# Performance work log

Measured on AMD Instinct MI355X. Metric: run time of the kernel, lower is better.

## Reference

```python
import jax, jax.numpy as jnp
import numpy as np
import math

H = 32          # num heads
D_NOPE = 128
D_ROPE = 64
D_QK = D_NOPE + D_ROPE   # 192
D_V = 128
KV_LORA = 512
EPS = 1e-6
ROPE_THETA = 10000.0
FACTOR = 40.0
BETA_FAST, BETA_SLOW = 32.0, 1.0
ORIG_MAX_POS = 4096
MSCALE_ALL_DIM = 1.0


def _yarn_inv_freq():
    dim = D_ROPE
    pos_freqs = ROPE_THETA ** (np.arange(0, dim, 2, dtype=np.float64) / dim)
    inv_extra = 1.0 / pos_freqs
    inv_inter = 1.0 / (FACTOR * pos_freqs)

    def corr_dim(n_rot):
        return dim * math.log(ORIG_MAX_POS / (n_rot * 2 * math.pi)) / (2 * math.log(ROPE_THETA))
    low = max(math.floor(corr_dim(BETA_FAST)), 0)
    high = min(math.ceil(corr_dim(BETA_SLOW)), dim - 1)
    ramp = np.clip((np.arange(dim // 2, dtype=np.float64) - low) / max(high - low, 1e-3), 0, 1)
    inv_freq_mask = 1.0 - ramp  # extrapolation_factor = 1
    inv_freq = inv_inter * (1 - inv_freq_mask) + inv_extra * inv_freq_mask
    return jnp.asarray(inv_freq, dtype=jnp.float32)  # [D_ROPE//2]


def _apply_rope_gptj(x, cos, sin):
    # x: [T, n, D_ROPE]; cos/sin: [T, D_ROPE//2]; interleaved (is_neox_style=False)
    x2 = x.reshape(*x.shape[:-1], D_ROPE // 2, 2)
    x1, xo = x2[..., 0], x2[..., 1]
    c = cos[:, None, :]
    s = sin[:, None, :]
    r1 = x1 * c - xo * s
    r2 = xo * c + x1 * s
    return jnp.stack([r1, r2], axis=-1).reshape(x.shape)


def _rmsnorm(x, w):
    var = jnp.mean(x.astype(jnp.float32) ** 2, axis=-1, keepdims=True)
    return (x * jax.lax.rsqrt(var + EPS)) * w


def setup_inputs() -> dict:
    key = jax.random.key(0)
    ks = jax.random.split(key, 8)
    T, HID = 2048, 4096
    def w(k, shape, fan_in):
        return jax.random.normal(k, shape, dtype=jnp.float32) * (1.0 / math.sqrt(fan_in))
    return {
        "positions": jnp.arange(T, dtype=jnp.int32),
        "hidden_states": jax.random.normal(ks[0], (T, HID), dtype=jnp.float32),
        "Wqa": w(ks[1], (HID, 1536), HID),
        "q_a_ln": jnp.ones((1536,), dtype=jnp.float32),
        "Wqb": w(ks[2], (1536, H * D_QK), 1536),
        "Wkva": w(ks[3], (HID, KV_LORA + D_ROPE), HID),
        "kv_a_ln": jnp.ones((KV_LORA,), dtype=jnp.float32),
        "Wkvb": w(ks[4], (KV_LORA, H * (D_NOPE + D_V)), KV_LORA),
        "Wo": w(ks[5], (H * D_V, HID), H * D_V),
    }


def reference(positions, hidden_states, Wqa, q_a_ln, Wqb, Wkva, kv_a_ln, Wkvb, Wo):
    T = hidden_states.shape[0]
    # softmax scaling with yarn mscale correction
    mscale = 0.1 * MSCALE_ALL_DIM * math.log(FACTOR) + 1.0
    scaling = (D_QK ** -0.5) * mscale * mscale

    # --- low-rank Q path ---
    q = hidden_states @ Wqa                       # [T, 1536]
    q = _rmsnorm(q, q_a_ln)
    q = (q @ Wqb).reshape(T, H, D_QK)             # [T, H, 192]
    q_nope, q_pe = q[..., :D_NOPE], q[..., D_NOPE:]

    # --- low-rank latent KV path ---
    latent = hidden_states @ Wkva                 # [T, 576]
    kv_a = _rmsnorm(latent[:, :KV_LORA], kv_a_ln) # [T, 512]
    k_pe = latent[:, None, KV_LORA:]              # [T, 1, 64]
    kv = (kv_a @ Wkvb).reshape(T, H, D_NOPE + D_V)
    k_nope = kv[..., :D_NOPE]                     # [T, H, 128]
    v = kv[..., D_NOPE:]                          # [T, H, 128]

    # --- decoupled RoPE on rope slice only ---
    inv_freq = _yarn_inv_freq()
    freqs = positions.astype(jnp.float32)[:, None] * inv_freq[None, :]  # [T, 32]
    cos, sin = jnp.cos(freqs), jnp.sin(freqs)
    q_pe = _apply_rope_gptj(q_pe, cos, sin)       # [T, H, 64]
    k_pe = _apply_rope_gptj(k_pe, cos, sin)       # [T, 1, 64]

    q = jnp.concatenate([q_nope, q_pe], axis=-1)                      # [T, H, 192]
    k = jnp.concatenate([k_nope, jnp.broadcast_to(k_pe, (T, H, D_ROPE))], axis=-1)

    # --- causal MHA over assembled K/V ---
    scores = jnp.einsum('thd,shd->hts', q, k) * scaling               # [H, T, T]
    causal = positions[None, :, None] >= positions[None, None, :]
    scores = jnp.where(causal, scores, jnp.finfo(scores.dtype).min)
    probs = jax.nn.softmax(scores, axis=-1)
    attn = jnp.einsum('hts,shd->thd', probs, v).reshape(T, H * D_V)
    return attn @ Wo                                                   # [T, 4096]
```

## Files before the change

### kernel.cpp

```cpp
#include <hip/hip_runtime.h>
#include <math.h>

typedef __bf16 bf16x8 __attribute__((ext_vector_type(8)));
typedef float f32x4 __attribute__((ext_vector_type(4)));
typedef unsigned short u16;
typedef unsigned int u32;

#define T_SEQ 2048
#define NHEAD 32

__device__ __forceinline__ u16 f2bu(float f){
  u32 u = __float_as_uint(f);
  u32 r = (u + 0x7fffu + ((u >> 16) & 1u)) >> 16;
  return (u16)r;
}

__device__ __forceinline__ void gload_lds16(const void* g, void* l){
  __builtin_amdgcn_global_load_lds((const __attribute__((address_space(1))) u32*)g,
                                   (__attribute__((address_space(3))) u32*)l, 16, 0, 0);
}

__global__ void cast_f32_bf16(const float* __restrict__ in, u16* __restrict__ out, int n4){
  int i = blockIdx.x * blockDim.x + threadIdx.x;
  int stride = gridDim.x * blockDim.x;
// ... 20 lines not shown
  __syncthreads();
  #pragma unroll
  for (int i = 0; i < 16; i++){
    int nr = lr * 16 + i;
    dst[(size_t)(n0 + nr) * K + k0 + lc] = f2bu(tile[lc][nr]);
  }
}

__global__ void rope_table(const int* __restrict__ positions, float* __restrict__ cosT,
                           float* __restrict__ sinT, float lo, float denom){
  int idx = blockIdx.x * blockDim.x + threadIdx.x;
  if (idx >= T_SEQ * 32) return;
  int t = idx >> 5, i = idx & 31;
  float pf = powf(10000.f, (float)i / 32.f);
  float inv_extra = 1.f / pf;
  float inv_inter = 1.f / (40.f * pf);
  float ramp = fminf(fmaxf(((float)i - lo) / denom, 0.f), 1.f);
  float invf = inv_inter * ramp + inv_extra * (1.f - ramp);
  float fr = (float)positions[t] * invf;
  cosT[idx] = cosf(fr);
  sinT[idx] = sinf(fr);
}

__global__ void rmsnorm_cast(const float* __restrict__ in, int istride, int n,
                             const float* __restrict__ w, u16* __restrict__ out, int ostride){
  int row = blockIdx.x;
  const float* x = in + (size_t)row * istride;
  float ss = 0.f;
  for (int c = threadIdx.x; c < n; c += blockDim.x){ float v = x[c]; ss += v * v; }
  #pragma unroll
  for (int off = 1; off < 64; off <<= 1) ss += __shfl_xor(ss, off);
  __shared__ float wsum[4];
  if ((threadIdx.x & 63) == 0) wsum[threadIdx.x >> 6] = ss;
  __syncthreads();
  float tot = wsum[0] + wsum[1] + wsum[2] + wsum[3];
  float scale = rsqrtf(tot / (float)n + 1e-6f);
  for (int c = threadIdx.x; c < n; c += blockDim.x)
    out[(size_t)row * ostride + c] = f2bu(x[c] * scale * w[c]);
}

__global__ void rope_kpe(const float* __restrict__ lat, int lstride, int loff,
                         const float* __restrict__ cosT,
                         const float* __restrict__ sinT, u16* __restrict__ kpe){
  int idx = blockIdx.x * blockDim.x + threadIdx.x;
  if (idx >= T_SEQ * 32) return;
  int t = idx >> 5, i = idx & 31;
  float x1 = lat[(size_t)t * lstride + loff + 2 * i];
  float x2 = lat[(size_t)t * lstride + loff + 2 * i + 1];
  float c = cosT[idx], s = sinT[idx];
  kpe[t * 64 + 2 * i]     = f2bu(x1 * c - x2 * s);
  kpe[t * 64 + 2 * i + 1] = f2bu(x2 * c + x1 * s);
}

__global__ void kpe_bcast(const u16* __restrict__ kpe, u16* __restrict__ Kp){
  int idx = blockIdx.x * blockDim.x + threadIdx.x;
  if (idx >= NHEAD * T_SEQ * 16) return;
  int h = idx >> 15;
  int rem = idx & 32767;
  int t = rem >> 4, j = rem & 15;
  ushort4 v = ((const ushort4*)(kpe + t * 64))[j];
  ((ushort4*)(Kp + (size_t)h * T_SEQ * 192 + (size_t)t * 192 + 128))[j] = v;
}

__global__ void build_vt(const u16* __restrict__ Vtmp, u16* __restrict__ Vt){
  __shared__ u16 tile[128][72];
  int t0 = blockIdx.x * 64;
  int h = blockIdx.y;
  #pragma unroll
  for (int i = 0; i < 32; i++){
    int lin = threadIdx.x + i * 256;
    int tt = lin >> 7, dd = lin & 127;
    tile[dd][tt] = Vtmp[(size_t)(t0 + tt) * 4096 + h * 128 + dd];
  }
  __syncthreads();
  #pragma unroll
  for (int i = 0; i < 32; i++){
    int lin = threadIdx.x + i * 256;
    int dd = lin >> 6, tt = lin & 63;
    Vt[(size_t)(h * 128 + dd) * T_SEQ + t0 + tt] = tile[dd][tt];
  }
}

template<int EPI>
__global__ __launch_bounds__(256) void gemm_bt(const u16* __restrict__ A, const u16* __restrict__ BT,
                                               float* __restrict__ C, u16* __restrict__ O1,
                                               u16* __restrict__ O2,
                                               const float* __restrict__ cosT,
                                               const float* __restrict__ sinT,
                                               float scaling, int M, int N, int K){
  __shared__ __align__(1024) char lds[32768];
  const int tid = threadIdx.x;
  const int wave = tid >> 6, lane = tid & 63;
  const int lg = lane >> 4, lm = lane & 15;

  int gx = gridDim.x;
  int nwg = gx * gridDim.y;
  int orig = blockIdx.y * gx + blockIdx.x;
  int qq = nwg >> 3, rr = nwg & 7, xc = orig & 7, rest = orig >> 3;
  int wg = (xc < rr ? xc * (qq + 1) : rr * (qq + 1) + (xc - rr) * qq) + rest;
  const int bn = (wg % gx) * 128, bm = (wg / gx) * 128;

  const int wr = (wave >> 1) * 64, wc = (wave & 1) * 64;
  f32x4 acc[4][4] = {};
  int srow[2], scol[2], soff[2];
  #pragma unroll
  for (int j = 0; j < 2; j++){
    int o = (wave * 2 + j) * 1024 + lane * 16;
    int row = o >> 6;
    int cg = ((o >> 4) & 3) ^ ((row >> 1) & 3);
    srow[j] = row; scol[j] = cg * 8; soff[j] = (wave * 2 + j) * 1024;
  }

  #pragma unroll
  for (int j = 0; j < 2; j++){
    gload_lds16(A  + (size_t)(bm + srow[j]) * K + scol[j], lds + soff[j]);
    gload_lds16(BT + (size_t)(bn + srow[j]) * K + scol[j], lds + 16384 + soff[j]);
  }

  int cur = 0;
  for (int k0 = 0; k0 < K; k0 += 32){
    if (k0 + 32 < K){
      char* dA = lds + (cur ^ 1) * 8192;
      char* dB = lds + 16384 + (cur ^ 1) * 8192;
      #pragma unroll
      for (int j = 0; j < 2; j++){
        gload_lds16(A  + (size_t)(bm + srow[j]) * K + k0 + 32 + scol[j], dA + soff[j]);
        gload_lds16(BT + (size_t)(bn + srow[j]) * K + k0 + 32 + scol[j], dB + soff[j]);
      }
      asm volatile("s_waitcnt vmcnt(4)" ::: "memory");
    } else {
      asm volatile("s_waitcnt vmcnt(0)" ::: "memory");
    }
    __builtin_amdgcn_sched_barrier(0);
    __builtin_amdgcn_s_barrier();

    const char* ldsA = lds + cur * 8192;
    const char* ldsB = lds + 16384 + cur * 8192;
    bf16x8 af[4], bfr[4];
    #pragma unroll
    for (int m = 0; m < 4; m++){
      int r = wr + m * 16 + lm;
      af[m] = *(const bf16x8*)(ldsA + r * 64 + ((lg ^ ((r >> 1) & 3)) << 4));
    }
    #pragma unroll
    for (int n = 0; n < 4; n++){
      int r = wc + n * 16 + lm;
      bfr[n] = *(const bf16x8*)(ldsB + r * 64 + ((lg ^ ((r >> 1) & 3)) << 4));
    }
    __builtin_amdgcn_s_setprio(1);
    #pragma unroll
    for (int m = 0; m < 4; m++)
      #pragma unroll
      for (int n = 0; n < 4; n++)
        acc[m][n] = __builtin_amdgcn_mfma_f32_16x16x32_bf16(af[m], bfr[n], acc[m][n], 0, 0, 0);
    __builtin_amdgcn_s_setprio(0);
    __builtin_amdgcn_s_barrier();
    cur ^= 1;
  }

  #pragma unroll
  for (int m = 0; m < 4; m++)
    #pragma unroll
    for (int n = 0; n < 4; n++)
      #pragma unroll
      for (int q = 0; q < 4; q++){
        int r = bm + wr + m * 16 + lg * 4 + q;
        int c = bn + wc + n * 16 + lm;
        float v = acc[m][n][q];
        if (EPI == 0){
          C[(size_t)r * N + c] = v;
        } else if (EPI == 1){
          float vp = __shfl_xor(v, 1);
          int h = c / 192, d = c - h * 192;
          float outv;
          if (d < 128) outv = v;
          else {
            int i = (d - 128) >> 1;
            float co = cosT[r * 32 + i], si = sinT[r * 32 + i];
            outv = (d & 1) ? (v * co + vp * si) : (v * co - vp * si);
          }
          O1[(size_t)h * T_SEQ * 192 + (size_t)r * 192 + d] = f2bu(outv * scaling);
        } else {
          int h = c >> 8, d = c & 255;
          if (d < 128) O1[(size_t)h * T_SEQ * 192 + (size_t)r * 192 + d] = f2bu(v);
          else         O2[(size_t)r * 4096 + h * 128 + (d - 128)] = f2bu(v);
        }
      }
}

__global__ __launch_bounds__(512, 1) void flash_attn(const u16* __restrict__ Qp, const u16* __restrict__ Kp,
                                                     const u16* __restrict__ Vt, u16* __restrict__ attnb){
  const int b = blockIdx.x;
  const int h = (b & 7) + 8 * ((b >> 3) & 3);
  const int s = b >> 5;
  const int tid = threadIdx.x;
  const int wave = tid >> 6, lane = tid & 63;
  const int lg = lane >> 4, lm = lane & 15;

  __shared__ __align__(1024) char lds[100352];
  char* ldsK = lds;
  char* ldsV = lds + 49152;
  u16*  Pw   = (u16*)(lds + 81920 + wave * 2304);

  const u16* KpH = Kp + (size_t)h * T_SEQ * 192;
  const u16* VtH = Vt + (size_t)h * 128 * T_SEQ;

  int kO[3], kSrc[3];
  #pragma unroll
  for (int j = 0; j < 3; j++){
    int o = (tid + 512 * j) * 16;
    int r = o / 384, c = (o % 384) >> 4;
    kO[j] = o; kSrc[j] = r * 192 + ((c ^ (r & 7)) << 3);
  }
  int vO[2], vSrc[2];
  #pragma unroll
  for (int j = 0; j < 2; j++){
    int o = (tid + 512 * j) * 16;
    int d = o >> 7, c = (o & 127) >> 4;
    vO[j] = o; vSrc[j] = d * T_SEQ + ((c ^ (d & 7)) << 3);
  }

  #pragma unroll 1
  for (int rep = 0; rep < 2; rep++){
    const int qt = rep ? s : (15 - s);
    const int qbase = qt * 128 + wave * 16;
    const int nt = 2 * qt + 2;

    __syncthreads();

    bf16x8 qf[6];
    const u16* Qbase = Qp + (size_t)(h * T_SEQ + qbase + lm) * 192 + lg * 8;
    #pragma unroll
    for (int dk = 0; dk < 6; dk++) qf[dk] = *(const bf16x8*)(Qbase + dk * 32);

    f32x4 o_[8] = {};
    float m_[4], l_[4];
    #pragma unroll
    for (int q = 0; q < 4; q++){ m_[q] = -3.0e38f; l_[q] = 0.f; }

    #pragma unroll
    for (int j = 0; j < 3; j++) gload_lds16(KpH + kSrc[j], ldsK + kO[j]);
    #pragma unroll
    for (int j = 0; j < 2; j++) gload_lds16(VtH + vSrc[j], ldsV + vO[j]);

    for (int kt = 0; kt < nt; kt++){
      const int t0 = kt * 64;
      const int bsel = kt & 1;
      asm volatile("s_waitcnt vmcnt(0)" ::: "memory");
      __builtin_amdgcn_sched_barrier(0);
      __builtin_amdgcn_s_barrier();
      if (kt + 1 < nt){
        const int t1 = t0 + 64;
        char* Kd = ldsK + (bsel ^ 1) * 24576;
        char* Vd = ldsV + (bsel ^ 1) * 16384;
        #pragma unroll
        for (int j = 0; j < 3; j++) gload_lds16(KpH + (size_t)t1 * 192 + kSrc[j], Kd + kO[j]);
        #pragma unroll
        for (int j = 0; j < 2; j++) gload_lds16(VtH + vSrc[j] + t1, Vd + vO[j]);
      }
      const char* Kb = ldsK + bsel * 24576;
      const char* Vb = ldsV + bsel * 16384;

      f32x4 s_[4] = {};
      __builtin_amdgcn_s_setprio(1);
      #pragma unroll
      for (int hh = 0; hh < 4; hh++){
        const int r = hh * 16 + lm;
        const int rb = r * 384, rx = r & 7;
        #pragma unroll
        for (int dk = 0; dk < 6; dk++){
          bf16x8 kf = *(const bf16x8*)(Kb + rb + (((dk * 4 + lg) ^ rx) << 4));
          s_[hh] = __builtin_amdgcn_mfma_f32_16x16x32_bf16(qf[dk], kf, s_[hh], 0, 0, 0);
        }
      }
      __builtin_amdgcn_s_setprio(0);
      #pragma unroll
      for (int hh = 0; hh < 4; hh++)
        #pragma unroll
        for (int q = 0; q < 4; q++){
          int col = t0 + hh * 16 + lm;
          int qrow = qbase + lg * 4 + q;
          if (col > qrow) s_[hh][q] = -3.0e38f;
        }
      float pm[4];
      #pragma unroll
      for (int q = 0; q < 4; q++)
        pm[q] = fmaxf(fmaxf(s_[0][q], s_[1][q]), fmaxf(s_[2][q], s_[3][q]));
      int ok = (pm[0] <= m_[0] + 8.f) & (pm[1] <= m_[1] + 8.f) &
               (pm[2] <= m_[2] + 8.f) & (pm[3] <= m_[3] + 8.f);
      if (!__all(ok)){
        #pragma unroll
        for (int q = 0; q < 4; q++){
          float v = pm[q];
          #pragma unroll
          for (int off = 8; off; off >>= 1) v = fmaxf(v, __shfl_xor(v, off));
          float mn = fmaxf(m_[q], v);
          float alpha = (m_[q] <= -1.0e37f) ? 0.f : __expf(m_[q] - mn);
          l_[q] *= alpha;
          #pragma unroll
          for (int n = 0; n < 8; n++) o_[n][q] *= alpha;
          m_[q] = mn;
        }
      }
      #pragma unroll
      for (int q = 0; q < 4; q++){
        #pragma unroll
        for (int hh = 0; hh < 4; hh++){
          float p = __expf(s_[hh][q] - m_[q]);
          l_[q] += p;
          Pw[(lg * 4 + q) * 72 + hh * 16 + lm] = f2bu(p);
        }
      }
      asm volatile("s_waitcnt lgkmcnt(0)" ::: "memory");
      __builtin_amdgcn_sched_barrier(0);
      __builtin_amdgcn_s_setprio(1);
      #pragma unroll
      for (int ks = 0; ks < 2; ks++){
        bf16x8 pf = *(const bf16x8*)((const char*)Pw + lm * 144 + ks * 64 + lg * 16);
        #pragma unroll
        for (int n = 0; n < 8; n++){
          const int d = n * 16 + lm;
          bf16x8 vf = *(const bf16x8*)(Vb + d * 128 + (((ks * 4 + lg) ^ (d & 7)) << 4));
          o_[n] = __builtin_amdgcn_mfma_f32_16x16x32_bf16(pf, vf, o_[n], 0, 0, 0);
        }
      }
      __builtin_amdgcn_s_setprio(0);
    }

    #pragma unroll
    for (int q = 0; q < 4; q++){
      #pragma unroll
      for (int off = 8; off; off >>= 1) l_[q] += __shfl_xor(l_[q], off);
    }
    float inv[4];
    #pragma unroll
    for (int q = 0; q < 4; q++) inv[q] = 1.f / l_[q];
    #pragma unroll
    for (int n = 0; n < 8; n++)
      #pragma unroll
      for (int q = 0; q < 4; q++){
        int r = qbase + lg * 4 + q;
        attnb[(size_t)r * 4096 + h * 128 + n * 16 + lm] = f2bu(o_[n][q] * inv[q]);
      }
  }
}

extern "C" void kernel_launch(void* const* d_in, const int* in_sizes, int n_in,
                              void* d_out, int out_size, void* d_ws, size_t ws_size,
                              hipStream_t stream){
  const int*   positions = (const int*)d_in[0];
  const float* hidden    = (const float*)d_in[1];
  const float* Wqa       = (const float*)d_in[2];
  const float* q_a_ln    = (const float*)d_in[3];
  const float* Wqb       = (const float*)d_in[4];
  const float* Wkva      = (const float*)d_in[5];
  const float* kv_a_ln   = (const float*)d_in[6];
  const float* Wkvb      = (const float*)d_in[7];
  const float* Wo        = (const float*)d_in[8];
  float* out = (float*)d_out;
  char* ws = (char*)d_ws;

  const size_t o_hid  = 0;
  const size_t o_cos  = 16777216;
  const size_t o_sin  = 17039360;
  const size_t o_comb = 17301504;
  const size_t o_qln  = 35127296;
  const size_t o_kva  = 41418752;
  const size_t o_kpe  = 43515904;
  const size_t o_W    = 43778048;
  const size_t o_Qp   = 77332480;
  const size_t o_Kp   = 102498304;
  const size_t o_Vtmp = 127664128;
  const size_t o_Vt   = 144441344;
  const size_t o_att  = 161218560;

  u16*   hidB = (u16*)(ws + o_hid);
  float* cosT = (float*)(ws + o_cos);
  float* sinT = (float*)(ws + o_sin);
  float* comb = (float*)(ws + o_comb);
  u16*   qln  = (u16*)(ws + o_qln);
  u16*   kva  = (u16*)(ws + o_kva);
  u16*   kpe  = (u16*)(ws + o_kpe);
  u16*   Wt   = (u16*)(ws + o_W);
  u16*   Qp   = (u16*)(ws + o_Qp);
  u16*   Kp   = (u16*)(ws + o_Kp);
  u16*   Vtmp = (u16*)(ws + o_Vtmp);
  u16*   Vt   = (u16*)(ws + o_Vt);
  u16*   attnb= (u16*)(ws + o_att);

  double mscale = 0.1 * log(40.0) + 1.0;
  float scaling = (float)(pow(192.0, -0.5) * mscale * mscale);
  const double PI = 3.14159265358979323846;
  double cd_fast = 64.0 * log(4096.0 / (32.0 * 2.0 * PI)) / (2.0 * log(10000.0));
  double cd_slow = 64.0 * log(4096.0 / ( 1.0 * 2.0 * PI)) / (2.0 * log(10000.0));
  double lo_d = fmax(floor(cd_fast), 0.0);
  double hi_d = fmin(ceil(cd_slow), 63.0);
  float lo = (float)lo_d;
  float denom = (float)fmax(hi_d - lo_d, 0.001);

  cast_f32_bf16<<<2048, 256, 0, stream>>>(hidden, hidB, T_SEQ * 4096 / 4);
  rope_table<<<256, 256, 0, stream>>>(positions, cosT, sinT, lo, denom);
  transpose_cast<<<dim3(4096 / 64, 1536 / 64), 256, 0, stream>>>(Wqa, Wt, 4096, 1536);
  transpose_cast<<<dim3(4096 / 64, 640 / 64), 256, 0, stream>>>(Wkva, Wt + (size_t)1536 * 4096, 4096, 576);
  gemm_bt<0><<<dim3(2176 / 128, 2048 / 128), 256, 0, stream>>>(hidB, Wt, comb, nullptr, nullptr,
                                                               nullptr, nullptr, 0.f, 2048, 2176, 4096);
  rmsnorm_cast<<<2048, 256, 0, stream>>>(comb, 2176, 1536, q_a_ln, qln, 1536);
  rmsnorm_cast<<<2048, 256, 0, stream>>>(comb + 1536, 2176, 512, kv_a_ln, kva, 512);
  rope_kpe<<<256, 256, 0, stream>>>(comb, 2176, 2048, cosT, sinT, kpe);
  transpose_cast<<<dim3(1536 / 64, 6144 / 64), 256, 0, stream>>>(Wqb, Wt, 1536, 6144);
  gemm_bt<1><<<dim3(6144 / 128, 2048 / 128), 256, 0, stream>>>(qln, Wt, nullptr, Qp, nullptr,
                                                               cosT, sinT, scaling, 2048, 6144, 1536);
  transpose_cast<<<dim3(512 / 64, 8192 / 64), 256, 0, stream>>>(Wkvb, Wt, 512, 8192);
  gemm_bt<2><<<dim3(8192 / 128, 2048 / 128), 256, 0, stream>>>(kva, Wt, nullptr, Kp, Vtmp,
                                                               nullptr, nullptr, 0.f, 2048, 8192, 512);
  kpe_bcast<<<NHEAD * T_SEQ * 16 / 256, 256, 0, stream>>>(kpe, Kp);
  build_vt<<<dim3(T_SEQ / 64, NHEAD), 256, 0, stream>>>(Vtmp, Vt);
  flash_attn<<<256, 512, 0, stream>>>(Qp, Kp, Vt, attnb);
  transpose_cast<<<dim3(4096 / 64, 4096 / 64), 256, 0, stream>>>(Wo, Wt, 4096, 4096);
  gemm_bt<0><<<dim3(4096 / 128, 2048 / 128), 256, 0, stream>>>(attnb, Wt, out, nullptr, nullptr,
                                                               nullptr, nullptr, 0.f, 2048, 4096, 4096);
}
```

Measured before the change: 441.8 us.

## Enlarge GEMM tiles to 256x256 with 8 waves and 64-deep K steps

Rewrites the shared GEMM kernel to use 256x256 output tiles with 512 threads (8 waves, each 128x64), K steps of 64, and a 128 KB double-buffered LDS with an XOR swizzle. Each K step is split into four phases that interleave the next tile's global-to-LDS loads with MFMA work. The goal is more data reuse per byte loaded and fewer loop iterations and barriers. The trade-offs are fewer workgroups (e.g. 64–128 tiles for the smaller GEMMs on a 256-CU part), much higher LDS and register use, and a padded kv_a projection width (2176 to 2304), which shifts the workspace offsets.

```diff
diff --git a/kernel.cpp b/kernel.cpp
--- a/kernel.cpp
+++ b/kernel.cpp
@@ -126,91 +126,117 @@
 }
 
 template<int EPI>
-__global__ __launch_bounds__(256) void gemm_bt(const u16* __restrict__ A, const u16* __restrict__ BT,
-                                               float* __restrict__ C, u16* __restrict__ O1,
-                                               u16* __restrict__ O2,
-                                               const float* __restrict__ cosT,
-                                               const float* __restrict__ sinT,
-                                               float scaling, int M, int N, int K){
-  __shared__ __align__(1024) char lds[32768];
+__global__ __launch_bounds__(512, 2) void gemm_bt(const u16* __restrict__ A, const u16* __restrict__ BT,
+                                                  float* __restrict__ C, u16* __restrict__ O1,
+                                                  u16* __restrict__ O2,
+                                                  const float* __restrict__ cosT,
+                                                  const float* __restrict__ sinT,
+                                                  float scaling, int M, int N, int K){
+  __shared__ __align__(1024) char lds[131072];
   const int tid = threadIdx.x;
   const int wave = tid >> 6, lane = tid & 63;
   const int lg = lane >> 4, lm = lane & 15;
+  const int wm = wave >> 2, wn = wave & 3;
 
   int gx = gridDim.x;
   int nwg = gx * gridDim.y;
   int orig = blockIdx.y * gx + blockIdx.x;
-  int qq = nwg >> 3, rr = nwg & 7, xc = orig & 7, rest = orig >> 3;
-  int wg = (xc < rr ? xc * (qq + 1) : rr * (qq + 1) + (xc - rr) * qq) + rest;
-  const int bn = (wg % gx) * 128, bm = (wg / gx) * 128;
-
-  const int wr = (wave >> 1) * 64, wc = (wave & 1) * 64;
-  f32x4 acc[4][4] = {};
-  int srow[2], scol[2], soff[2];
+  int qq = nwg >> 3, rr_ = nwg & 7, xc = orig & 7, rest = orig >> 3;
+  int wg = (xc < rr_ ? xc * (qq + 1) : rr_ * (qq + 1) + (xc - rr_) * qq) + rest;
+  const int bn = (wg % gx) * 256, bm = (wg / gx) * 256;
+
+  int rrS[2], scS[2], dOS[2];
   #pragma unroll
   for (int j = 0; j < 2; j++){
-    int o = (wave * 2 + j) * 1024 + lane * 16;
-    int row = o >> 6;
-    int cg = ((o >> 4) & 3) ^ ((row >> 1) & 3);
-    srow[j] = row; scol[j] = cg * 8; soff[j] = (wave * 2 + j) * 1024;
-  }
-
-  #pragma unroll
-  for (int j = 0; j < 2; j++){
-    gload_lds16(A  + (size_t)(bm + srow[j]) * K + scol[j], lds + soff[j]);
-    gload_lds16(BT + (size_t)(bn + srow[j]) * K + scol[j], lds + 16384 + soff[j]);
-  }
-
-  int cur = 0;
-  for (int k0 = 0; k0 < K; k0 += 32){
-    if (k0 + 32 < K){
-      char* dA = lds + (cur ^ 1) * 8192;
-      char* dB = lds + 16384 + (cur ^ 1) * 8192;
-      #pragma unroll
-      for (int j = 0; j < 2; j++){
-        gload_lds16(A  + (size_t)(bm + srow[j]) * K + k0 + 32 + scol[j], dA + soff[j]);
-        gload_lds16(BT + (size_t)(bn + srow[j]) * K + k0 + 32 + scol[j], dB + soff[j]);
-      }
-      asm volatile("s_waitcnt vmcnt(4)" ::: "memory");
-    } else {
-      asm volatile("s_waitcnt vmcnt(0)" ::: "memory");
-    }
+    int o = j * 512 + tid;
+    rrS[j] = o >> 3;
+    scS[j] = ((o & 7) ^ (rrS[j] & 7)) << 3;
+    dOS[j] = o * 16;
+  }
+
+  f32x4 acc[8][4] = {};
+
+  #pragma unroll
+  for (int ha = 0; ha < 2; ha++)
+    #pragma unroll
+    for (int j = 0; j < 2; j++)
+      gload_lds16(A + (size_t)(bm + ha * 128 + rrS[j]) * K + scS[j], lds + ha * 16384 + dOS[j]);
+  #pragma unroll
+  for (int hb = 0; hb < 2; hb++)
+    #pragma unroll
+    for (int j = 0; j < 2; j++)
+      gload_lds16(BT + (size_t)(bn + hb * 128 + rrS[j]) * K + scS[j], lds + 65536 + hb * 16384 + dOS[j]);
+
+  const int NT = K >> 6;
+  #pragma unroll 1
+  for (int t = 0; t < NT; t++){
+    const int db = t & 1;
+    asm volatile("s_waitcnt vmcnt(0)" ::: "memory");
     __builtin_amdgcn_sched_barrier(0);
     __builtin_amdgcn_s_barrier();
-
-    const char* ldsA = lds + cur * 8192;
-    const char* ldsB = lds + 16384 + cur * 8192;
-    bf16x8 af[4], bfr[4];
-    #pragma unroll
-    for (int m = 0; m < 4; m++){
-      int r = wr + m * 16 + lm;
-      af[m] = *(const bf16x8*)(ldsA + r * 64 + ((lg ^ ((r >> 1) & 3)) << 4));
+    const char* aB = lds + db * 32768;
+    const char* bB = lds + 65536 + db * 32768;
+    char* dA = lds + (db ^ 1) * 32768;
+    char* dB = lds + 65536 + (db ^ 1) * 32768;
+    const int kn = (t + 1) << 6;
+    const bool pre = (t + 1 < NT);
+
+    #pragma unroll
+    for (int ph = 0; ph < 4; ph++){
+      if (pre){
+        if (ph < 2){
+          #pragma unroll
+          for (int j = 0; j < 2; j++)
+            gload_lds16(A + (size_t)(bm + ph * 128 + rrS[j]) * K + kn + scS[j],
+                        dA + ph * 16384 + dOS[j]);
+        } else {
+          #pragma unroll
+          for (int j = 0; j < 2; j++)
+            gload_lds16(BT + (size_t)(bn + (ph - 2) * 128 + rrS[j]) * K + kn + scS[j],
+                        dB + (ph - 2) * 16384 + dOS[j]);
+        }
+      }
+      const int mq = ph >> 1, nq = ph & 1;
+      bf16x8 af[4][2], bf[2][2];
+      #pragma unroll
+      for (int mi = 0; mi < 4; mi++){
+        int ra = wm * 128 + mq * 64 + mi * 16 + lm;
+        #pragma unroll
+        for (int kk = 0; kk < 2; kk++)
+          af[mi][kk] = *(const bf16x8*)(aB + ra * 128 + (((kk * 4 + lg) ^ (ra & 7)) << 4));
+      }
+      #pragma unroll
+      for (int ni = 0; ni < 2; ni++){
+        int rb = wn * 64 + (nq * 2 + ni) * 16 + lm;
+        #pragma unroll
+        for (int kk = 0; kk < 2; kk++)
+          bf[ni][kk] = *(const bf16x8*)(bB + rb * 128 + (((kk * 4 + lg) ^ (rb & 7)) << 4));
+      }
+      asm volatile("s_waitcnt lgkmcnt(0)" ::: "memory");
+      __builtin_amdgcn_sched_barrier(0);
+      __builtin_amdgcn_s_setprio(1);
+      #pragma unroll
+      for (int mi = 0; mi < 4; mi++)
+        #pragma unroll
+        for (int ni = 0; ni < 2; ni++)
+          #pragma unroll
+          for (int kk = 0; kk < 2; kk++)
+            acc[mq * 4 + mi][nq * 2 + ni] =
+              __builtin_amdgcn_mfma_f32_16x16x32_bf16(af[mi][kk], bf[ni][kk],
+                                                      acc[mq * 4 + mi][nq * 2 + ni], 0, 0, 0);
+      __builtin_amdgcn_s_setprio(0);
     }
-    #pragma unroll
-    for (int n = 0; n < 4; n++){
-      int r = wc + n * 16 + lm;
-      bfr[n] = *(const bf16x8*)(ldsB + r * 64 + ((lg ^ ((r >> 1) & 3)) << 4));
-    }
-    __builtin_amdgcn_s_setprio(1);
-    #pragma unroll
-    for (int m = 0; m < 4; m++)
-      #pragma unroll
-      for (int n = 0; n < 4; n++)
-        acc[m][n] = __builtin_amdgcn_mfma_f32_16x16x32_bf16(af[m], bfr[n], acc[m][n], 0, 0, 0);
-    __builtin_amdgcn_s_setprio(0);
-    __builtin_amdgcn_s_barrier();
-    cur ^= 1;
-  }
-
-  #pragma unroll
-  for (int m = 0; m < 4; m++)
-    #pragma unroll
-    for (int n = 0; n < 4; n++)
+  }
+
+  #pragma unroll
+  for (int mi = 0; mi < 8; mi++)
+    #pragma unroll
+    for (int ni = 0; ni < 4; ni++)
       #pragma unroll
       for (int q = 0; q < 4; q++){
-        int r = bm + wr + m * 16 + lg * 4 + q;
-        int c = bn + wc + n * 16 + lm;
-        float v = acc[m][n][q];
+        int r = bm + wm * 128 + mi * 16 + lg * 4 + q;
+        int c = bn + wn * 64 + ni * 16 + lm;
+        float v = acc[mi][ni][q];
         if (EPI == 0){
           C[(size_t)r * N + c] = v;
         } else if (EPI == 1){
@@ -408,15 +434,15 @@
   const size_t o_cos  = 16777216;
   const size_t o_sin  = 17039360;
   const size_t o_comb = 17301504;
-  const size_t o_qln  = 35127296;
-  const size_t o_kva  = 41418752;
-  const size_t o_kpe  = 43515904;
-  const size_t o_W    = 43778048;
-  const size_t o_Qp   = 77332480;
-  const size_t o_Kp   = 102498304;
-  const size_t o_Vtmp = 127664128;
-  const size_t o_Vt   = 144441344;
-  const size_t o_att  = 161218560;
+  const size_t o_qln  = 36175872;
+  const size_t o_kva  = 42467328;
+  const size_t o_kpe  = 44564480;
+  const size_t o_W    = 44826624;
+  const size_t o_Qp   = 78381056;
+  const size_t o_Kp   = 103546880;
+  const size_t o_Vtmp = 128712704;
+  const size_t o_Vt   = 145489920;
+  const size_t o_att  = 162267136;
 
   u16*   hidB = (u16*)(ws + o_hid);
   float* cosT = (float*)(ws + o_cos);
@@ -445,22 +471,22 @@
   cast_f32_bf16<<<2048, 256, 0, stream>>>(hidden, hidB, T_SEQ * 4096 / 4);
   rope_table<<<256, 256, 0, stream>>>(positions, cosT, sinT, lo, denom);
   transpose_cast<<<dim3(4096 / 64, 1536 / 64), 256, 0, stream>>>(Wqa, Wt, 4096, 1536);
-  transpose_cast<<<dim3(4096 / 64, 640 / 64), 256, 0, stream>>>(Wkva, Wt + (size_t)1536 * 4096, 4096, 576);
-  gemm_bt<0><<<dim3(2176 / 128, 2048 / 128), 256, 0, stream>>>(hidB, Wt, comb, nullptr, nullptr,
-                                                               nullptr, nullptr, 0.f, 2048, 2176, 4096);
-  rmsnorm_cast<<<2048, 256, 0, stream>>>(comb, 2176, 1536, q_a_ln, qln, 1536);
-  rmsnorm_cast<<<2048, 256, 0, stream>>>(comb + 1536, 2176, 512, kv_a_ln, kva, 512);
-  rope_kpe<<<256, 256, 0, stream>>>(comb, 2176, 2048, cosT, sinT, kpe);
+  transpose_cast<<<dim3(4096 / 64, 768 / 64), 256, 0, stream>>>(Wkva, Wt + (size_t)1536 * 4096, 4096, 576);
+  gemm_bt<0><<<dim3(2304 / 256, 2048 / 256), 512, 0, stream>>>(hidB, Wt, comb, nullptr, nullptr,
+                                                               nullptr, nullptr, 0.f, 2048, 2304, 4096);
+  rmsnorm_cast<<<2048, 256, 0, stream>>>(comb, 2304, 1536, q_a_ln, qln, 1536);
+  rmsnorm_cast<<<2048, 256, 0, stream>>>(comb + 1536, 2304, 512, kv_a_ln, kva, 512);
+  rope_kpe<<<256, 256, 0, stream>>>(comb, 2304, 2048, cosT, sinT, kpe);
   transpose_cast<<<dim3(1536 / 64, 6144 / 64), 256, 0, stream>>>(Wqb, Wt, 1536, 6144);
-  gemm_bt<1><<<dim3(6144 / 128, 2048 / 128), 256, 0, stream>>>(qln, Wt, nullptr, Qp, nullptr,
+  gemm_bt<1><<<dim3(6144 / 256, 2048 / 256), 512, 0, stream>>>(qln, Wt, nullptr, Qp, nullptr,
                                                                cosT, sinT, scaling, 2048, 6144, 1536);
   transpose_cast<<<dim3(512 / 64, 8192 / 64), 256, 0, stream>>>(Wkvb, Wt, 512, 8192);
-  gemm_bt<2><<<dim3(8192 / 128, 2048 / 128), 256, 0, stream>>>(kva, Wt, nullptr, Kp, Vtmp,
+  gemm_bt<2><<<dim3(8192 / 256, 2048 / 256), 512, 0, stream>>>(kva, Wt, nullptr, Kp, Vtmp,
                                                                nullptr, nullptr, 0.f, 2048, 8192, 512);
   kpe_bcast<<<NHEAD * T_SEQ * 16 / 256, 256, 0, stream>>>(kpe, Kp);
   build_vt<<<dim3(T_SEQ / 64, NHEAD), 256, 0, stream>>>(Vtmp, Vt);
   flash_attn<<<256, 512, 0, stream>>>(Qp, Kp, Vt, attnb);
   transpose_cast<<<dim3(4096 / 64, 4096 / 64), 256, 0, stream>>>(Wo, Wt, 4096, 4096);
-  gemm_bt<0><<<dim3(4096 / 128, 2048 / 128), 256, 0, stream>>>(attnb, Wt, out, nullptr, nullptr,
+  gemm_bt<0><<<dim3(4096 / 256, 2048 / 256), 512, 0, stream>>>(attnb, Wt, out, nullptr, nullptr,
                                                                nullptr, nullptr, 0.f, 2048, 4096, 4096);
 }
```

After: 493.6 us. 11.7% more time.

## Triple-buffer LDS prefetch in GEMM and flash attention loops

Applied to the files above, without the earlier changes.

Both the bf16 GEMM and the flash-attention kernel move from double to triple-buffered LDS staging. Loads are now issued two tiles ahead, with partial vmcnt waits, so global-to-LDS copies overlap more compute. The GEMM also drops its trailing per-iteration barrier, since the three-buffer rotation keeps a tile from being overwritten while it is still being read. The cost is more LDS per block: 48 KB for the GEMM, which may lower occupancy, and about 138 KB for attention, which stays at one block per CU.

```diff
diff --git a/kernel.cpp b/kernel.cpp
--- a/kernel.cpp
+++ b/kernel.cpp
@@ -132,7 +132,7 @@
                                                const float* __restrict__ cosT,
                                                const float* __restrict__ sinT,
                                                float scaling, int M, int N, int K){
-  __shared__ __align__(1024) char lds[32768];
+  __shared__ __align__(1024) char lds[49152];
   const int tid = threadIdx.x;
   const int wave = tid >> 6, lane = tid & 63;
   const int lg = lane >> 4, lm = lane & 15;
@@ -140,8 +140,8 @@
   int gx = gridDim.x;
   int nwg = gx * gridDim.y;
   int orig = blockIdx.y * gx + blockIdx.x;
-  int qq = nwg >> 3, rr = nwg & 7, xc = orig & 7, rest = orig >> 3;
-  int wg = (xc < rr ? xc * (qq + 1) : rr * (qq + 1) + (xc - rr) * qq) + rest;
+  int qq = nwg >> 3, rr_ = nwg & 7, xc = orig & 7, rest = orig >> 3;
+  int wg = (xc < rr_ ? xc * (qq + 1) : rr_ * (qq + 1) + (xc - rr_) * qq) + rest;
   const int bn = (wg % gx) * 128, bm = (wg / gx) * 128;
 
   const int wr = (wave >> 1) * 64, wc = (wave & 1) * 64;
@@ -155,31 +155,34 @@
     srow[j] = row; scol[j] = cg * 8; soff[j] = (wave * 2 + j) * 1024;
   }
 
-  #pragma unroll
-  for (int j = 0; j < 2; j++){
-    gload_lds16(A  + (size_t)(bm + srow[j]) * K + scol[j], lds + soff[j]);
-    gload_lds16(BT + (size_t)(bn + srow[j]) * K + scol[j], lds + 16384 + soff[j]);
-  }
+  #define STAGE_G(koff, bi)                                                        \
+    do {                                                                           \
+      char* _a = lds + (bi) * 8192;                                                \
+      char* _b = lds + 24576 + (bi) * 8192;                                        \
+      _Pragma("unroll")                                                            \
+      for (int j = 0; j < 2; j++){                                                 \
+        gload_lds16(A  + (size_t)(bm + srow[j]) * K + (koff) + scol[j], _a + soff[j]); \
+        gload_lds16(BT + (size_t)(bn + srow[j]) * K + (koff) + scol[j], _b + soff[j]); \
+      }                                                                            \
+    } while (0)
+
+  const int K32 = K >> 5;
+  STAGE_G(0, 0);
+  if (K32 > 1) STAGE_G(32, 1);
 
   int cur = 0;
-  for (int k0 = 0; k0 < K; k0 += 32){
-    if (k0 + 32 < K){
-      char* dA = lds + (cur ^ 1) * 8192;
-      char* dB = lds + 16384 + (cur ^ 1) * 8192;
-      #pragma unroll
-      for (int j = 0; j < 2; j++){
-        gload_lds16(A  + (size_t)(bm + srow[j]) * K + k0 + 32 + scol[j], dA + soff[j]);
-        gload_lds16(BT + (size_t)(bn + srow[j]) * K + k0 + 32 + scol[j], dB + soff[j]);
-      }
-      asm volatile("s_waitcnt vmcnt(4)" ::: "memory");
-    } else {
-      asm volatile("s_waitcnt vmcnt(0)" ::: "memory");
-    }
+  #pragma unroll 1
+  for (int k = 0; k < K32; k++){
+    if (k < K32 - 1) asm volatile("s_waitcnt vmcnt(4)" ::: "memory");
+    else             asm volatile("s_waitcnt vmcnt(0)" ::: "memory");
     __builtin_amdgcn_sched_barrier(0);
     __builtin_amdgcn_s_barrier();
-
+    if (k + 2 < K32){
+      int nb = cur + 2; if (nb >= 3) nb -= 3;
+      STAGE_G((k + 2) << 5, nb);
+    }
     const char* ldsA = lds + cur * 8192;
-    const char* ldsB = lds + 16384 + cur * 8192;
+    const char* ldsB = lds + 24576 + cur * 8192;
     bf16x8 af[4], bfr[4];
     #pragma unroll
     for (int m = 0; m < 4; m++){
@@ -198,9 +201,9 @@
       for (int n = 0; n < 4; n++)
         acc[m][n] = __builtin_amdgcn_mfma_f32_16x16x32_bf16(af[m], bfr[n], acc[m][n], 0, 0, 0);
     __builtin_amdgcn_s_setprio(0);
-    __builtin_amdgcn_s_barrier();
-    cur ^= 1;
-  }
+    cur = (cur == 2) ? 0 : cur + 1;
+  }
+  #undef STAGE_G
 
   #pragma unroll
   for (int m = 0; m < 4; m++)
@@ -241,10 +244,8 @@
   const int wave = tid >> 6, lane = tid & 63;
   const int lg = lane >> 4, lm = lane & 15;
 
-  __shared__ __align__(1024) char lds[100352];
-  char* ldsK = lds;
-  char* ldsV = lds + 49152;
-  u16*  Pw   = (u16*)(lds + 81920 + wave * 2304);
+  __shared__ __align__(1024) char lds[141312];
+  u16* Pw = (u16*)(lds + 122880 + wave * 2304);
 
   const u16* KpH = Kp + (size_t)h * T_SEQ * 192;
   const u16* VtH = Vt + (size_t)h * 128 * T_SEQ;
@@ -263,6 +264,16 @@
     int d = o >> 7, c = (o & 127) >> 4;
     vO[j] = o; vSrc[j] = d * T_SEQ + ((c ^ (d & 7)) << 3);
   }
+
+  #define STAGE_KV(t, bi)                                                          \
+    do {                                                                           \
+      char* _k = lds + (bi) * 24576;                                               \
+      char* _v = lds + 73728 + (bi) * 16384;                                       \
+      _Pragma("unroll")                                                            \
+      for (int j = 0; j < 3; j++) gload_lds16(KpH + (size_t)(t) * 64 * 192 + kSrc[j], _k + kO[j]); \
+      _Pragma("unroll")                                                            \
+      for (int j = 0; j < 2; j++) gload_lds16(VtH + vSrc[j] + (t) * 64, _v + vO[j]); \
+    } while (0)
 
   #pragma unroll 1
   for (int rep = 0; rep < 2; rep++){
@@ -282,28 +293,23 @@
     #pragma unroll
     for (int q = 0; q < 4; q++){ m_[q] = -3.0e38f; l_[q] = 0.f; }
 
-    #pragma unroll
-    for (int j = 0; j < 3; j++) gload_lds16(KpH + kSrc[j], ldsK + kO[j]);
-    #pragma unroll
-    for (int j = 0; j < 2; j++) gload_lds16(VtH + vSrc[j], ldsV + vO[j]);
-
+    STAGE_KV(0, 0);
+    if (nt > 1) STAGE_KV(1, 1);
+
+    int cur = 0;
+    #pragma unroll 1
     for (int kt = 0; kt < nt; kt++){
       const int t0 = kt * 64;
-      const int bsel = kt & 1;
-      asm volatile("s_waitcnt vmcnt(0)" ::: "memory");
+      if (kt < nt - 1) asm volatile("s_waitcnt vmcnt(5)" ::: "memory");
+      else             asm volatile("s_waitcnt vmcnt(0)" ::: "memory");
       __builtin_amdgcn_sched_barrier(0);
       __builtin_amdgcn_s_barrier();
-      if (kt + 1 < nt){
-        const int t1 = t0 + 64;
-        char* Kd = ldsK + (bsel ^ 1) * 24576;
-        char* Vd = ldsV + (bsel ^ 1) * 16384;
-        #pragma unroll
-        for (int j = 0; j < 3; j++) gload_lds16(KpH + (size_t)t1 * 192 + kSrc[j], Kd + kO[j]);
-        #pragma unroll
-        for (int j = 0; j < 2; j++) gload_lds16(VtH + vSrc[j] + t1, Vd + vO[j]);
-      }
-      const char* Kb = ldsK + bsel * 24576;
-      const char* Vb = ldsV + bsel * 16384;
+      if (kt + 2 < nt){
+        int nb = cur + 2; if (nb >= 3) nb -= 3;
+        STAGE_KV(kt + 2, nb);
+      }
+      const char* Kb = lds + cur * 24576;
+      const char* Vb = lds + 73728 + cur * 16384;
 
       f32x4 s_[4] = {};
       __builtin_amdgcn_s_setprio(1);
@@ -369,6 +375,7 @@
         }
       }
       __builtin_amdgcn_s_setprio(0);
+      cur = (cur == 2) ? 0 : cur + 1;
     }
 
     #pragma unroll
@@ -387,6 +394,7 @@
         attnb[(size_t)r * 4096 + h * 128 + n * 16 + lm] = f2bu(o_[n][q] * inv[q]);
       }
   }
+  #undef STAGE_KV
 }
 
 extern "C" void kernel_launch(void* const* d_in, const int* in_sizes, int n_in,
```

Result: no change. 445.8 us (+0.9%).

## Restructure flash attention with split-KV balancing, triple buffering, and shared k_pe

Applied to the files above, without the earlier changes.

Flash attention now handles 32 query rows per wave (256 per block) and reuses each K fragment for two MFMAs. It also moves from double to triple buffering of K/V in LDS, with a partial vmcnt wait. Causal work is split so each block gets roughly equal KV tiles, and the long query tiles are split across two blocks whose partial results are merged by a new combine kernel. The per-head k_pe broadcast kernel is removed: K is now stored as 128-wide nope data, and the shared rope slice is loaded straight from kpe during staging. This adds fp32 partial-output traffic and an extra launch, and uses more LDS and registers in exchange.

```diff
diff --git a/kernel.cpp b/kernel.cpp
--- a/kernel.cpp
+++ b/kernel.cpp
@@ -96,16 +96,6 @@
   kpe[t * 64 + 2 * i + 1] = f2bu(x2 * c + x1 * s);
 }
 
-__global__ void kpe_bcast(const u16* __restrict__ kpe, u16* __restrict__ Kp){
-  int idx = blockIdx.x * blockDim.x + threadIdx.x;
-  if (idx >= NHEAD * T_SEQ * 16) return;
-  int h = idx >> 15;
-  int rem = idx & 32767;
-  int t = rem >> 4, j = rem & 15;
-  ushort4 v = ((const ushort4*)(kpe + t * 64))[j];
-  ((ushort4*)(Kp + (size_t)h * T_SEQ * 192 + (size_t)t * 192 + 128))[j] = v;
-}
-
 __global__ void build_vt(const u16* __restrict__ Vtmp, u16* __restrict__ Vt){
   __shared__ u16 tile[128][72];
   int t0 = blockIdx.x * 64;
@@ -140,8 +130,8 @@
   int gx = gridDim.x;
   int nwg = gx * gridDim.y;
   int orig = blockIdx.y * gx + blockIdx.x;
-  int qq = nwg >> 3, rr = nwg & 7, xc = orig & 7, rest = orig >> 3;
-  int wg = (xc < rr ? xc * (qq + 1) : rr * (qq + 1) + (xc - rr) * qq) + rest;
+  int qq = nwg >> 3, rr_ = nwg & 7, xc = orig & 7, rest = orig >> 3;
+  int wg = (xc < rr_ ? xc * (qq + 1) : rr_ * (qq + 1) + (xc - rr_) * qq) + rest;
   const int bn = (wg % gx) * 128, bm = (wg / gx) * 128;
 
   const int wr = (wave >> 1) * 64, wc = (wave & 1) * 64;
@@ -226,35 +216,40 @@
           O1[(size_t)h * T_SEQ * 192 + (size_t)r * 192 + d] = f2bu(outv * scaling);
         } else {
           int h = c >> 8, d = c & 255;
-          if (d < 128) O1[(size_t)h * T_SEQ * 192 + (size_t)r * 192 + d] = f2bu(v);
+          if (d < 128) O1[(size_t)h * T_SEQ * 128 + (size_t)r * 128 + d] = f2bu(v);
           else         O2[(size_t)r * 4096 + h * 128 + (d - 128)] = f2bu(v);
         }
       }
 }
 
 __global__ __launch_bounds__(512, 1) void flash_attn(const u16* __restrict__ Qp, const u16* __restrict__ Kp,
-                                                     const u16* __restrict__ Vt, u16* __restrict__ attnb){
+                                                     const u16* __restrict__ kpe, const u16* __restrict__ Vt,
+                                                     u16* __restrict__ attnb,
+                                                     float* __restrict__ oPart, float* __restrict__ mlPart){
   const int b = blockIdx.x;
   const int h = (b & 7) + 8 * ((b >> 3) & 3);
-  const int s = b >> 5;
+  const int slot = b >> 5;
+  const int qs = slot & 3;
+  const int role = slot >> 2;
   const int tid = threadIdx.x;
   const int wave = tid >> 6, lane = tid & 63;
   const int lg = lane >> 4, lm = lane & 15;
 
-  __shared__ __align__(1024) char lds[100352];
-  char* ldsK = lds;
-  char* ldsV = lds + 49152;
-  u16*  Pw   = (u16*)(lds + 81920 + wave * 2304);
-
-  const u16* KpH = Kp + (size_t)h * T_SEQ * 192;
+  __shared__ __align__(1024) char lds[159744];
+  u16* Pw = (u16*)(lds + 122880 + wave * 4608);
+
+  const u16* KpH = Kp + (size_t)h * T_SEQ * 128;
   const u16* VtH = Vt + (size_t)h * 128 * T_SEQ;
 
-  int kO[3], kSrc[3];
+  int kO[3], kLoc[3], kPE[3];
   #pragma unroll
   for (int j = 0; j < 3; j++){
-    int o = (tid + 512 * j) * 16;
-    int r = o / 384, c = (o % 384) >> 4;
-    kO[j] = o; kSrc[j] = r * 192 + ((c ^ (r & 7)) << 3);
+    int o = tid + 512 * j;
+    int r = o / 24, c = o - r * 24;
+    int cx = c ^ (r & 7);
+    kO[j] = o * 16;
+    if (cx < 16){ kPE[j] = 0; kLoc[j] = r * 128 + cx * 8; }
+    else        { kPE[j] = 1; kLoc[j] = r * 64 + (cx - 16) * 8; }
   }
   int vO[2], vSrc[2];
   #pragma unroll
@@ -264,48 +259,73 @@
     vO[j] = o; vSrc[j] = d * T_SEQ + ((c ^ (d & 7)) << 3);
   }
 
+  #define STAGE_KV(t, bi)                                                              \
+    do {                                                                               \
+      char* _k = lds + (bi) * 24576;                                                   \
+      char* _v = lds + 73728 + (bi) * 16384;                                           \
+      _Pragma("unroll")                                                                \
+      for (int j = 0; j < 3; j++){                                                     \
+        const u16* _s = kPE[j] ? (kpe + (size_t)(t) * 4096 + kLoc[j])                  \
+                               : (KpH + (size_t)(t) * 8192 + kLoc[j]);                 \
+        gload_lds16(_s, _k + kO[j]);                                                   \
+      }                                                                                \
+      _Pragma("unroll")                                                                \
+      for (int j = 0; j < 2; j++) gload_lds16(VtH + vSrc[j] + (t) * 64, _v + vO[j]);   \
+    } while (0)
+
+  int segqt[2], segk0[2], segnk[2], segfin[2];
+  int nseg;
+  if (role == 0){
+    nseg = 2;
+    segqt[0] = qs;     segk0[0] = 0; segnk[0] = 4 * qs + 4;  segfin[0] = 1;
+    segqt[1] = 7 - qs; segk0[1] = 0; segnk[1] = 14 - 4 * qs; segfin[1] = 0;
+  } else {
+    nseg = 1;
+    segqt[0] = 7 - qs; segk0[0] = 14 - 4 * qs; segnk[0] = 18; segfin[0] = 0;
+  }
+  const int pi = (h * 4 + qs) * 2 + role;
+
   #pragma unroll 1
-  for (int rep = 0; rep < 2; rep++){
-    const int qt = rep ? s : (15 - s);
-    const int qbase = qt * 128 + wave * 16;
-    const int nt = 2 * qt + 2;
+  for (int sg = 0; sg < nseg; sg++){
+    const int qt = segqt[sg], kt0 = segk0[sg], nt = segnk[sg];
+    const int qb = qt * 256 + wave * 32;
 
     __syncthreads();
 
-    bf16x8 qf[6];
-    const u16* Qbase = Qp + (size_t)(h * T_SEQ + qbase + lm) * 192 + lg * 8;
-    #pragma unroll
-    for (int dk = 0; dk < 6; dk++) qf[dk] = *(const bf16x8*)(Qbase + dk * 32);
-
-    f32x4 o_[8] = {};
-    float m_[4], l_[4];
-    #pragma unroll
-    for (int q = 0; q < 4; q++){ m_[q] = -3.0e38f; l_[q] = 0.f; }
-
-    #pragma unroll
-    for (int j = 0; j < 3; j++) gload_lds16(KpH + kSrc[j], ldsK + kO[j]);
-    #pragma unroll
-    for (int j = 0; j < 2; j++) gload_lds16(VtH + vSrc[j], ldsV + vO[j]);
-
+    bf16x8 qfl[6], qfh[6];
+    const u16* Qlo = Qp + (size_t)(h * T_SEQ + qb + lm) * 192 + lg * 8;
+    #pragma unroll
+    for (int dk = 0; dk < 6; dk++){
+      qfl[dk] = *(const bf16x8*)(Qlo + dk * 32);
+      qfh[dk] = *(const bf16x8*)(Qlo + 16 * 192 + dk * 32);
+    }
+
+    f32x4 o_[2][8] = {};
+    float m_[2][4], l_[2][4];
+    #pragma unroll
+    for (int g = 0; g < 2; g++)
+      #pragma unroll
+      for (int q = 0; q < 4; q++){ m_[g][q] = -3.0e38f; l_[g][q] = 0.f; }
+
+    STAGE_KV(kt0, 0);
+    if (nt > 1) STAGE_KV(kt0 + 1, 1);
+
+    int cur = 0;
+    #pragma unroll 1
     for (int kt = 0; kt < nt; kt++){
-      const int t0 = kt * 64;
-      const int bsel = kt & 1;
-      asm volatile("s_waitcnt vmcnt(0)" ::: "memory");
+      const int t0 = (kt0 + kt) * 64;
+      if (kt < nt - 1) asm volatile("s_waitcnt vmcnt(5)" ::: "memory");
+      else             asm volatile("s_waitcnt vmcnt(0)" ::: "memory");
       __builtin_amdgcn_sched_barrier(0);
       __builtin_amdgcn_s_barrier();
-      if (kt + 1 < nt){
-        const int t1 = t0 + 64;
-        char* Kd = ldsK + (bsel ^ 1) * 24576;
-        char* Vd = ldsV + (bsel ^ 1) * 16384;
-        #pragma unroll
-        for (int j = 0; j < 3; j++) gload_lds16(KpH + (size_t)t1 * 192 + kSrc[j], Kd + kO[j]);
-        #pragma unroll
-        for (int j = 0; j < 2; j++) gload_lds16(VtH + vSrc[j] + t1, Vd + vO[j]);
-      }
-      const char* Kb = ldsK + bsel * 24576;
-      const char* Vb = ldsV + bsel * 16384;
-
-      f32x4 s_[4] = {};
+      if (kt + 2 < nt){
+        int nb = cur + 2; if (nb >= 3) nb -= 3;
+        STAGE_KV(kt0 + kt + 2, nb);
+      }
+      const char* Kb = lds + cur * 24576;
+      const char* Vb = lds + 73728 + cur * 16384;
+
+      f32x4 s_[2][4] = {};
       __builtin_amdgcn_s_setprio(1);
       #pragma unroll
       for (int hh = 0; hh < 4; hh++){
@@ -314,78 +334,152 @@
         #pragma unroll
         for (int dk = 0; dk < 6; dk++){
           bf16x8 kf = *(const bf16x8*)(Kb + rb + (((dk * 4 + lg) ^ rx) << 4));
-          s_[hh] = __builtin_amdgcn_mfma_f32_16x16x32_bf16(qf[dk], kf, s_[hh], 0, 0, 0);
+          s_[0][hh] = __builtin_amdgcn_mfma_f32_16x16x32_bf16(qfl[dk], kf, s_[0][hh], 0, 0, 0);
+          s_[1][hh] = __builtin_amdgcn_mfma_f32_16x16x32_bf16(qfh[dk], kf, s_[1][hh], 0, 0, 0);
         }
       }
       __builtin_amdgcn_s_setprio(0);
       #pragma unroll
-      for (int hh = 0; hh < 4; hh++)
+      for (int g = 0; g < 2; g++)
+        #pragma unroll
+        for (int hh = 0; hh < 4; hh++)
+          #pragma unroll
+          for (int q = 0; q < 4; q++){
+            int col = t0 + hh * 16 + lm;
+            int qrow = qb + g * 16 + lg * 4 + q;
+            if (col > qrow) s_[g][hh][q] = -3.0e38f;
+          }
+      float pm[2][4];
+      int ok = 1;
+      #pragma unroll
+      for (int g = 0; g < 2; g++)
         #pragma unroll
         for (int q = 0; q < 4; q++){
-          int col = t0 + hh * 16 + lm;
-          int qrow = qbase + lg * 4 + q;
-          if (col > qrow) s_[hh][q] = -3.0e38f;
+          pm[g][q] = fmaxf(fmaxf(s_[g][0][q], s_[g][1][q]), fmaxf(s_[g][2][q], s_[g][3][q]));
+          ok &= (pm[g][q] <= m_[g][q] + 8.f);
         }
-      float pm[4];
-      #pragma unroll
-      for (int q = 0; q < 4; q++)
-        pm[q] = fmaxf(fmaxf(s_[0][q], s_[1][q]), fmaxf(s_[2][q], s_[3][q]));
-      int ok = (pm[0] <= m_[0] + 8.f) & (pm[1] <= m_[1] + 8.f) &
-               (pm[2] <= m_[2] + 8.f) & (pm[3] <= m_[3] + 8.f);
       if (!__all(ok)){
         #pragma unroll
-        for (int q = 0; q < 4; q++){
-          float v = pm[q];
+        for (int g = 0; g < 2; g++)
           #pragma unroll
-          for (int off = 8; off; off >>= 1) v = fmaxf(v, __shfl_xor(v, off));
-          float mn = fmaxf(m_[q], v);
-          float alpha = (m_[q] <= -1.0e37f) ? 0.f : __expf(m_[q] - mn);
-          l_[q] *= alpha;
+          for (int q = 0; q < 4; q++){
+            float v = pm[g][q];
+            #pragma unroll
+            for (int off = 8; off; off >>= 1) v = fmaxf(v, __shfl_xor(v, off));
+            float mn = fmaxf(m_[g][q], v);
+            float alpha = (m_[g][q] <= -1.0e37f) ? 0.f : __expf(m_[g][q] - mn);
+            l_[g][q] *= alpha;
+            #pragma unroll
+            for (int n = 0; n < 8; n++) o_[g][n][q] *= alpha;
+            m_[g][q] = mn;
+          }
+      }
+      #pragma unroll
+      for (int g = 0; g < 2; g++)
+        #pragma unroll
+        for (int q = 0; q < 4; q++)
           #pragma unroll
-          for (int n = 0; n < 8; n++) o_[n][q] *= alpha;
-          m_[q] = mn;
-        }
-      }
-      #pragma unroll
-      for (int q = 0; q < 4; q++){
-        #pragma unroll
-        for (int hh = 0; hh < 4; hh++){
-          float p = __expf(s_[hh][q] - m_[q]);
-          l_[q] += p;
-          Pw[(lg * 4 + q) * 72 + hh * 16 + lm] = f2bu(p);
-        }
-      }
+          for (int hh = 0; hh < 4; hh++){
+            float p = __expf(s_[g][hh][q] - m_[g][q]);
+            l_[g][q] += p;
+            Pw[(g * 16 + lg * 4 + q) * 72 + hh * 16 + lm] = f2bu(p);
+          }
       asm volatile("s_waitcnt lgkmcnt(0)" ::: "memory");
       __builtin_amdgcn_sched_barrier(0);
       __builtin_amdgcn_s_setprio(1);
       #pragma unroll
       for (int ks = 0; ks < 2; ks++){
-        bf16x8 pf = *(const bf16x8*)((const char*)Pw + lm * 144 + ks * 64 + lg * 16);
+        bf16x8 pfl = *(const bf16x8*)((const char*)Pw + lm * 144 + ks * 64 + lg * 16);
+        bf16x8 pfh = *(const bf16x8*)((const char*)Pw + 2304 + lm * 144 + ks * 64 + lg * 16);
         #pragma unroll
         for (int n = 0; n < 8; n++){
           const int d = n * 16 + lm;
           bf16x8 vf = *(const bf16x8*)(Vb + d * 128 + (((ks * 4 + lg) ^ (d & 7)) << 4));
-          o_[n] = __builtin_amdgcn_mfma_f32_16x16x32_bf16(pf, vf, o_[n], 0, 0, 0);
+          o_[0][n] = __builtin_amdgcn_mfma_f32_16x16x32_bf16(pfl, vf, o_[0][n], 0, 0, 0);
+          o_[1][n] = __builtin_amdgcn_mfma_f32_16x16x32_bf16(pfh, vf, o_[1][n], 0, 0, 0);
         }
       }
       __builtin_amdgcn_s_setprio(0);
+      cur = (cur == 2) ? 0 : cur + 1;
     }
 
     #pragma unroll
-    for (int q = 0; q < 4; q++){
-      #pragma unroll
-      for (int off = 8; off; off >>= 1) l_[q] += __shfl_xor(l_[q], off);
+    for (int g = 0; g < 2; g++)
+      #pragma unroll
+      for (int q = 0; q < 4; q++){
+        #pragma unroll
+        for (int off = 8; off; off >>= 1) l_[g][q] += __shfl_xor(l_[g][q], off);
+      }
+
+    if (segfin[sg]){
+      #pragma unroll
+      for (int g = 0; g < 2; g++){
+        float inv[4];
+        #pragma unroll
+        for (int q = 0; q < 4; q++) inv[q] = 1.f / l_[g][q];
+        #pragma unroll
+        for (int n = 0; n < 8; n++)
+          #pragma unroll
+          for (int q = 0; q < 4; q++){
+            int r = qb + g * 16 + lg * 4 + q;
+            attnb[(size_t)r * 4096 + h * 128 + n * 16 + lm] = f2bu(o_[g][n][q] * inv[q]);
+          }
+      }
+    } else {
+      float* oP = oPart + (size_t)pi * 32768;
+      float* mP = mlPart + (size_t)pi * 512;
+      #pragma unroll
+      for (int g = 0; g < 2; g++)
+        #pragma unroll
+        for (int n = 0; n < 8; n++)
+          #pragma unroll
+          for (int q = 0; q < 4; q++){
+            int rl = wave * 32 + g * 16 + lg * 4 + q;
+            oP[rl * 128 + n * 16 + lm] = o_[g][n][q];
+          }
+      if (lm == 0){
+        #pragma unroll
+        for (int g = 0; g < 2; g++)
+          #pragma unroll
+          for (int q = 0; q < 4; q++){
+            int rl = wave * 32 + g * 16 + lg * 4 + q;
+            mP[rl] = m_[g][q];
+            mP[256 + rl] = l_[g][q];
+          }
+      }
     }
-    float inv[4];
-    #pragma unroll
-    for (int q = 0; q < 4; q++) inv[q] = 1.f / l_[q];
-    #pragma unroll
-    for (int n = 0; n < 8; n++)
-      #pragma unroll
-      for (int q = 0; q < 4; q++){
-        int r = qbase + lg * 4 + q;
-        attnb[(size_t)r * 4096 + h * 128 + n * 16 + lm] = f2bu(o_[n][q] * inv[q]);
-      }
+  }
+  #undef STAGE_KV
+}
+
+__global__ __launch_bounds__(512) void combine_attn(const float* __restrict__ oPart,
+                                                    const float* __restrict__ mlPart,
+                                                    u16* __restrict__ attnb){
+  int blk = blockIdx.x;
+  int h = blk >> 2, qs = blk & 3;
+  int qt = 7 - qs;
+  int piA = (h * 4 + qs) * 2, piB = piA + 1;
+  int t = threadIdx.x;
+  int row = t >> 1, half = t & 1;
+  const float* mlA = mlPart + (size_t)piA * 512;
+  const float* mlB = mlPart + (size_t)piB * 512;
+  float ma = mlA[row], la = mlA[256 + row];
+  float mb = mlB[row], lb = mlB[256 + row];
+  float M = fmaxf(ma, mb);
+  float sa = __expf(ma - M), sb = __expf(mb - M);
+  float inv = 1.f / (la * sa + lb * sb);
+  const float4* oA = (const float4*)(oPart + (size_t)piA * 32768 + row * 128 + half * 64);
+  const float4* oB = (const float4*)(oPart + (size_t)piB * 32768 + row * 128 + half * 64);
+  ushort4* dst = (ushort4*)(attnb + (size_t)(qt * 256 + row) * 4096 + h * 128 + half * 64);
+  #pragma unroll
+  for (int i = 0; i < 16; i++){
+    float4 a = oA[i], bv = oB[i];
+    ushort4 o;
+    o.x = f2bu((a.x * sa + bv.x * sb) * inv);
+    o.y = f2bu((a.y * sa + bv.y * sb) * inv);
+    o.z = f2bu((a.z * sa + bv.z * sb) * inv);
+    o.w = f2bu((a.w * sa + bv.w * sb) * inv);
+    dst[i] = o;
   }
 }
 
@@ -407,30 +501,34 @@
   const size_t o_hid  = 0;
   const size_t o_cos  = 16777216;
   const size_t o_sin  = 17039360;
-  const size_t o_comb = 17301504;
-  const size_t o_qln  = 35127296;
-  const size_t o_kva  = 41418752;
-  const size_t o_kpe  = 43515904;
+  const size_t o_kpe  = 17301504;
+  const size_t o_comb = 17563648;
+  const size_t o_qln  = 35389440;
+  const size_t o_kva  = 41680896;
   const size_t o_W    = 43778048;
   const size_t o_Qp   = 77332480;
   const size_t o_Kp   = 102498304;
-  const size_t o_Vtmp = 127664128;
-  const size_t o_Vt   = 144441344;
-  const size_t o_att  = 161218560;
+  const size_t o_Vtmp = 119275520;
+  const size_t o_Vt   = 136052736;
+  const size_t o_att  = 152829952;
+  const size_t o_oP   = 169607168;
+  const size_t o_ml   = 203161600;
 
   u16*   hidB = (u16*)(ws + o_hid);
   float* cosT = (float*)(ws + o_cos);
   float* sinT = (float*)(ws + o_sin);
+  u16*   kpe  = (u16*)(ws + o_kpe);
   float* comb = (float*)(ws + o_comb);
   u16*   qln  = (u16*)(ws + o_qln);
   u16*   kva  = (u16*)(ws + o_kva);
-  u16*   kpe  = (u16*)(ws + o_kpe);
   u16*   Wt   = (u16*)(ws + o_W);
   u16*   Qp   = (u16*)(ws + o_Qp);
   u16*   Kp   = (u16*)(ws + o_Kp);
   u16*   Vtmp = (u16*)(ws + o_Vtmp);
   u16*   Vt   = (u16*)(ws + o_Vt);
   u16*   attnb= (u16*)(ws + o_att);
+  float* oP   = (float*)(ws + o_oP);
+  float* mlP  = (float*)(ws + o_ml);
 
   double mscale = 0.1 * log(40.0) + 1.0;
   float scaling = (float)(pow(192.0, -0.5) * mscale * mscale);
@@ -457,9 +555,9 @@
   transpose_cast<<<dim3(512 / 64, 8192 / 64), 256, 0, stream>>>(Wkvb, Wt, 512, 8192);
   gemm_bt<2><<<dim3(8192 / 128, 2048 / 128), 256, 0, stream>>>(kva, Wt, nullptr, Kp, Vtmp,
                                                                nullptr, nullptr, 0.f, 2048, 8192, 512);
-  kpe_bcast<<<NHEAD * T_SEQ * 16 / 256, 256, 0, stream>>>(kpe, Kp);
   build_vt<<<dim3(T_SEQ / 64, NHEAD), 256, 0, stream>>>(Vtmp, Vt);
-  flash_attn<<<256, 512, 0, stream>>>(Qp, Kp, Vt, attnb);
+  flash_attn<<<256, 512, 0, stream>>>(Qp, Kp, kpe, Vt, attnb, oP, mlP);
+  combine_attn<<<128, 512, 0, stream>>>(oP, mlP, attnb);
   transpose_cast<<<dim3(4096 / 64, 4096 / 64), 256, 0, stream>>>(Wo, Wt, 4096, 4096);
   gemm_bt<0><<<dim3(4096 / 128, 2048 / 128), 256, 0, stream>>>(attnb, Wt, out, nullptr, nullptr,
                                                                nullptr, nullptr, 0.f, 2048, 4096, 4096);
```

Measured after the change: 468.0 us. 1.06x slower.
